# Optimization experiments

Measured on AMD Instinct MI355X. Metric: run time of the kernel, lower is better.

The kernel has to match this reference:

```python
import jax, jax.numpy as jnp
import numpy as np

N = 20000; E = 320000; B = 512
F_IN = 43; HID = 128; H = 4; C = 128  # TransformerConv: out_channels=128, heads=4 -> H*C=512
SCALE = float(1.0 / np.sqrt(C))


def _lin(key, nin, nout):
    k1, k2 = jax.random.split(key)
    W = jax.random.normal(k1, (nin, nout), jnp.float32) * 0.05
    b = jax.random.normal(k2, (nout,), jnp.float32) * 0.05
    return W, b


def setup_inputs() -> dict:
    key = jax.random.key(0)
    ks = jax.random.split(key, 64)
    inp = {}
    inp['x'] = jax.random.normal(ks[0], (N, F_IN), jnp.float32)
    inp['edge_index'] = jax.random.randint(ks[1], (2, E), 0, N, jnp.int32)
    inp['batch'] = jnp.sort(jax.random.randint(ks[2], (N,), 0, B, jnp.int32))
    i = 3
    for l, din in enumerate([F_IN, HID, HID], start=1):
        for nm in ['q', 'k', 'v', 's']:
            W, b = _lin(ks[i], din, H * C); i += 1
            inp['W%s%d' % (nm, l)] = W
            inp['b%s%d' % (nm, l)] = b
        W, b = _lin(ks[i], H * C, HID); i += 1
        inp['Wm%d' % l] = W; inp['bm%d' % l] = b
    inp['Wg1'], inp['bg1'] = _lin(ks[i], 2 * HID, 1024); i += 1
    inp['Wg2'], inp['bg2'] = _lin(ks[i], 1024, 512); i += 1
    inp['Wf1'], inp['bf1'] = _lin(ks[i], 512, 256); i += 1
    inp['Wf2'], inp['bf2'] = _lin(ks[i], 256, 1); i += 1
    return inp


def _tconv(x, src, dst, Wq, bq, Wk, bk, Wv, bv, Ws, bs):
    # PyG TransformerConv (concat=True, root_weight=True, eval -> no dropout)
    n = x.shape[0]
    q = (x @ Wq + bq).reshape(n, H, C)
    k = (x @ Wk + bk).reshape(n, H, C)
    v = (x @ Wv + bv).reshape(n, H, C)
    alpha = jnp.einsum('ehc,ehc->eh', q[dst], k[src]) * SCALE  # [E, H]
    amax = jax.ops.segment_max(alpha, dst, num_segments=n)
    amax = jnp.where(jnp.isfinite(amax), amax, 0.0)
    ex = jnp.exp(alpha - amax[dst])
    den = jax.ops.segment_sum(ex, dst, num_segments=n)
    w = ex / jnp.maximum(den[dst], 1e-16)  # segment softmax over incoming edges
    agg = jax.ops.segment_sum(w[:, :, None] * v[src], dst, num_segments=n)
    return agg.reshape(n, H * C) + x @ Ws + bs


def reference(x, edge_index, batch,
              Wq1, bq1, Wk1, bk1, Wv1, bv1, Ws1, bs1, Wm1, bm1,
              Wq2, bq2, Wk2, bk2, Wv2, bv2, Ws2, bs2, Wm2, bm2,
              Wq3, bq3, Wk3, bk3, Wv3, bv3, Ws3, bs3, Wm3, bm3,
              Wg1, bg1, Wg2, bg2, Wf1, bf1, Wf2, bf2):
    src, dst = edge_index[0], edge_index[1]
    layers = [
        (Wq1, bq1, Wk1, bk1, Wv1, bv1, Ws1, bs1, Wm1, bm1),
        (Wq2, bq2, Wk2, bk2, Wv2, bv2, Ws2, bs2, Wm2, bm2),
        (Wq3, bq3, Wk3, bk3, Wv3, bv3, Ws3, bs3, Wm3, bm3),
    ]
    h = x
    for (Wq, bq, Wk, bk, Wv, bv, Ws, bs, Wm, bm) in layers:
        h = jax.nn.relu(_tconv(h, src, dst, Wq, bq, Wk, bk, Wv, bv, Ws, bs) @ Wm + bm)
    # global max pool + global mean pool over graphs
    gm = jax.ops.segment_max(h, batch, num_segments=B)
    gm = jnp.where(jnp.isfinite(gm), gm, 0.0)
    cnt = jax.ops.segment_sum(jnp.ones((h.shape[0], 1), h.dtype), batch, num_segments=B)
    ga = jax.ops.segment_sum(h, batch, num_segments=B) / jnp.maximum(cnt, 1.0)
    g = jnp.concatenate([gm, ga], axis=1)  # [B, 256]
    g = jax.nn.relu(g @ Wg1 + bg1)
    g = jax.nn.relu(g @ Wg2 + bg2)
    g = jax.nn.relu(g @ Wf1 + bf1)
    return g @ Wf2 + bf2  # [B, 1]
```

## Files before the change

### kernel.cpp

```cpp
#include <hip/hip_runtime.h>
#include <hip/hip_bf16.h>
#include <hip/hip_fp16.h>
#include <math.h>

#define NN 20000
#define MPAD 20096
#define NE 320000
#define NB 512
#define FIN 43
#define HD 128
#define HC 512
#define ATT_SCALE 0.08838834764831843f

typedef __attribute__((ext_vector_type(8))) _Float16 f16x8v;
typedef __attribute__((ext_vector_type(8))) short short8v;
typedef __attribute__((ext_vector_type(4))) float f32x4v;
typedef _Float16 half2_t __attribute__((ext_vector_type(2)));

__device__ __forceinline__ void gload16(void* lds, const void* g) {
  __builtin_amdgcn_global_load_lds(
      (const __attribute__((address_space(1))) void*)g,
      (__attribute__((address_space(3))) void*)lds, 16, 0, 0);
}

__device__ __forceinline__ float dot2acc(half2_t a, half2_t b, float c) {
#if __has_builtin(__builtin_amdgcn_fdot2)
  return __builtin_amdgcn_fdot2(a, b, c, false);
#else
  return c + (float)a[0] * (float)b[0] + (float)a[1] * (float)b[1];
#endif
}

__global__ __launch_bounds__(256, 2) void gemm_qkv_kernel(
    const __half* __restrict__ A_, int ldA,
    const __half* __restrict__ B_,
    const float* __restrict__ bias,
    __half* __restrict__ qh16, __half* __restrict__ kvh,
    int M, int K)
{
  __shared__ _Float16 Ah[128 * 64], Bh[128 * 64];
  const _Float16* A = (const _Float16*)A_;
  const _Float16* B = (const _Float16*)B_;
  const int tid = threadIdx.x;
  const int w = tid >> 6, lane = tid & 63;
  const int rowBase = blockIdx.y * 128, colBase = blockIdx.x * 128;
  const int srow = lane >> 3;
  const int sw = ((lane & 7) ^ srow) << 3;
  const int lr = lane & 15, lg = lane >> 4;
  const int wr = w >> 1, wc = w & 1;

  f32x4v acc[4][4];
#pragma unroll
  for (int m = 0; m < 4; ++m)
#pragma unroll
    for (int n = 0; n < 4; ++n) acc[m][n] = (f32x4v){0.f, 0.f, 0.f, 0.f};

  for (int k0 = 0; k0 < K; k0 += 64) {
    if (k0) __syncthreads();
#pragma unroll
    for (int t = 0; t < 4; ++t) {
      int r0 = w * 32 + t * 8;
      size_t arow = (size_t)(rowBase + r0 + srow) * ldA + k0 + sw;
      size_t brow = (size_t)(colBase + r0 + srow) * K + k0 + sw;
      gload16(&Ah[r0 * 64], A + arow);
      gload16(&Bh[r0 * 64], B + brow);
    }
    __syncthreads();
#pragma unroll
    for (int kk = 0; kk < 2; ++kk) {
      f16x8v ah[4], bh[4];
      int cbase = ((kk * 4 + lg) ^ (lr & 7)) * 8;
#pragma unroll
      for (int m = 0; m < 4; ++m)
        ah[m] = *(const f16x8v*)&Ah[(wr * 64 + m * 16 + lr) * 64 + cbase];
#pragma unroll
      for (int n = 0; n < 4; ++n)
        bh[n] = *(const f16x8v*)&Bh[(wc * 64 + n * 16 + lr) * 64 + cbase];
#pragma unroll
      for (int m = 0; m < 4; ++m)
#pragma unroll
        for (int n = 0; n < 4; ++n)
          acc[m][n] = __builtin_amdgcn_mfma_f32_16x16x32_f16(ah[m], bh[n], acc[m][n], 0, 0, 0);
    }
  }
#pragma unroll
  for (int m = 0; m < 4; ++m) {
#pragma unroll
    for (int n = 0; n < 4; ++n) {
      int col = colBase + wc * 64 + n * 16 + lr;
      float bb = bias[col];
#pragma unroll
      for (int r = 0; r < 4; ++r) {
        int row = rowBase + wr * 64 + m * 16 + lg * 4 + r;
        if (row < M) {
          float v = acc[m][n][r] + bb;
          if (col < 512) {
            qh16[(size_t)row * 512 + col] = __float2half(v);
          } else if (col < 1024) {
            int cc = col - 512;
            kvh[(size_t)row * 1024 + (cc >> 7) * 256 + (cc & 127)] = __float2half(v);
          } else {
            int cc = col - 1024;
            kvh[(size_t)row * 1024 + (cc >> 7) * 256 + 128 + (cc & 127)] = __float2half(v);
          }
        }
      }
    }
  }
}

__global__ __launch_bounds__(256, 2) void gemm64_kernel(
    const __half* __restrict__ A_, int ldA, int Ksplit,
    const __half* __restrict__ A2_, int ldA2,
    const __half* __restrict__ B_,
    const float* __restrict__ bias,
    float* __restrict__ Y, int ldY,
    __half* __restrict__ Yh,
    int M, int K)
{
  __shared__ _Float16 Ah[64 * 64], Bh[128 * 64];
  const _Float16* B = (const _Float16*)B_;
  const int tid = threadIdx.x;
  const int w = tid >> 6, lane = tid & 63;
  const int rowBase = blockIdx.x * 64, colBase = blockIdx.y * 128;
  const int srow = lane >> 3;
  const int sw = ((lane & 7) ^ srow) << 3;
  const int lr = lane & 15, lg = lane >> 4;
  const int wr = w >> 1, wc = w & 1;

  f32x4v acc[2][4];
#pragma unroll
  for (int m = 0; m < 2; ++m)
#pragma unroll
    for (int n = 0; n < 4; ++n) acc[m][n] = (f32x4v){0.f, 0.f, 0.f, 0.f};

  for (int k0 = 0; k0 < K; k0 += 64) {
    if (k0) __syncthreads();
    const _Float16* sA;
    int ldS, kloc;
    if (k0 < Ksplit) { sA = (const _Float16*)A_;  ldS = ldA;  kloc = k0; }
    else             { sA = (const _Float16*)A2_; ldS = ldA2; kloc = k0 - Ksplit; }
#pragma unroll
    for (int t = 0; t < 2; ++t) {
      int r0 = w * 16 + t * 8;
      size_t arow = (size_t)(rowBase + r0 + srow) * ldS + kloc + sw;
      gload16(&Ah[r0 * 64], sA + arow);
    }
#pragma unroll
    for (int t = 0; t < 4; ++t) {
      int r0 = w * 32 + t * 8;
      size_t brow = (size_t)(colBase + r0 + srow) * K + k0 + sw;
      gload16(&Bh[r0 * 64], B + brow);
    }
    __syncthreads();
#pragma unroll
    for (int kk = 0; kk < 2; ++kk) {
      f16x8v ah[2], bh[4];
      int cbase = ((kk * 4 + lg) ^ (lr & 7)) * 8;
#pragma unroll
      for (int m = 0; m < 2; ++m)
        ah[m] = *(const f16x8v*)&Ah[(wr * 32 + m * 16 + lr) * 64 + cbase];
#pragma unroll
      for (int n = 0; n < 4; ++n)
        bh[n] = *(const f16x8v*)&Bh[(wc * 64 + n * 16 + lr) * 64 + cbase];
#pragma unroll
      for (int m = 0; m < 2; ++m)
#pragma unroll
        for (int n = 0; n < 4; ++n)
          acc[m][n] = __builtin_amdgcn_mfma_f32_16x16x32_f16(ah[m], bh[n], acc[m][n], 0, 0, 0);
    }
  }
#pragma unroll
  for (int m = 0; m < 2; ++m) {
#pragma unroll
    for (int n = 0; n < 4; ++n) {
      int col = colBase + wc * 64 + n * 16 + lr;
      float bb = bias[col];
#pragma unroll
      for (int r = 0; r < 4; ++r) {
        int row = rowBase + wr * 32 + m * 16 + lg * 4 + r;
        if (row < M) {
          float v = fmaxf(acc[m][n][r] + bb, 0.f);
          if (Y) Y[(size_t)row * ldY + col] = v;
          Yh[(size_t)row * ldY + col] = __float2half(v);
        }
      }
    }
  }
}

struct WsmArgs {
  const float* Ws[3];
  const float* Wm[3];
  const float* bs[3];
  const float* bm[3];
  __half* Wmx[3];
  float* bm2;
};

__global__ __launch_bounds__(256) void wsm_kernel(WsmArgs a)
{
  int idx = blockIdx.x * 256 + threadIdx.x;
  if (idx < 3 * 128 * 128) {
    int l = idx >> 14, r = idx & 16383;
    int n = r >> 7, d = r & 127;
    int K2pad = (l == 0) ? 64 : 128;
    if (d >= K2pad) return;
    int din = (l == 0) ? FIN : 128;
    float v = 0.f;
    if (d < din) {
      const float* ws = a.Ws[l] + (size_t)d * 512;
      const float* wm = a.Wm[l];
      for (int j = 0; j < 512; ++j) v += ws[j] * wm[(size_t)j * 128 + n];
    }
    int KP = 512 + K2pad;
    a.Wmx[l][(size_t)n * KP + 512 + d] = __float2half(v);
  } else {
    int r = idx - 3 * 128 * 128;
    if (r >= 384) return;
    int l = r >> 7, n = r & 127;
    float v = a.bm[l][n];
    const float* bs = a.bs[l];
    const float* wm = a.Wm[l];
    for (int j = 0; j < 512; ++j) v += bs[j] * wm[(size_t)j * 128 + n];
    a.bm2[l * 128 + n] = v;
  }
}

struct PackArgs {
  const float* W[9];
  const float* b[9];
  const float* Wm[3];
  const float *Wg1, *Wg2, *Wf1;
  __half* Wp[3];
  __half* Wmx[3];
  __half *Wg1p, *Wg2p, *Wf1p;
  float* bpack;
};

__global__ __launch_bounds__(256) void pack_all_kernel(PackArgs a)
{
  int idx = blockIdx.x * 256 + threadIdx.x;
  if (idx < 98304) {
    int n = idx >> 6, k = idx & 63;
    int mat = n >> 9, nn = n & 511;
    float v = (k < FIN) ? a.W[mat][(size_t)k * 512 + nn] : 0.f;
    a.Wp[0][idx] = __float2half(v);
  } else if (idx < 491520) {
    int rel = idx - 98304;
    int l = 1 + rel / 196608;
    int r2 = rel % 196608;
    int n = r2 >> 7, k = r2 & 127;
    int mat = n >> 9, nn = n & 511;
    a.Wp[l][r2] = __float2half(a.W[l * 3 + mat][(size_t)k * 512 + nn]);
  } else if (idx < 688128) {
    int rel = idx - 491520;
    int l = rel >> 16;
    int r2 = rel & 65535;
    int n = r2 >> 9, k = r2 & 511;
    int KP = (l == 0) ? 576 : 640;
    a.Wmx[l][(size_t)n * KP + k] = __float2half(a.Wm[l][(size_t)k * 128 + n]);
  } else if (idx < 692736) {
    int rel = idx - 688128;
    int l = rel / 1536, c = rel % 1536;
    a.bpack[rel] = a.b[l * 3 + (c >> 9)][c & 511];
  } else if (idx < 954880) {
    int rel = idx - 692736;
    int n = rel >> 8, k = rel & 255;
    a.Wg1p[rel] = __float2half(a.Wg1[(size_t)k * 1024 + n]);
  } else if (idx < 1479168) {
    int rel = idx - 954880;
    int n = rel >> 10, k = rel & 1023;
    a.Wg2p[rel] = __float2half(a.Wg2[(size_t)k * 512 + n]);
  } else if (idx < 1610240) {
    int rel = idx - 1479168;
    int n = rel >> 9, k = rel & 511;
    a.Wf1p[rel] = __float2half(a.Wf1[(size_t)k * 256 + n]);
  }
}

__global__ __launch_bounds__(256) void split_x_kernel(
    const float* __restrict__ x, __half* __restrict__ xh)
{
  int idx = blockIdx.x * 256 + threadIdx.x;
  if (idx >= NN * 64) return;
  int r = idx >> 6, c = idx & 63;
  float v = (c < FIN) ? x[(size_t)r * FIN + c] : 0.f;
  xh[idx] = __float2half(v);
}

__global__ __launch_bounds__(256) void count_kernel(const int* __restrict__ dst, int* __restrict__ cnt)
{
  int e = blockIdx.x * 256 + threadIdx.x;
  if (e < NE) atomicAdd(&cnt[dst[e]], 1);
}

__global__ __launch_bounds__(1024) void scan_kernel(const int* __restrict__ cnt, int* __restrict__ row_start)
{
  __shared__ int sums[1024];
  int t = threadIdx.x;
  const int per = (NN + 1023) / 1024;
  int beg = t * per;
  int end = beg + per; if (end > NN) end = NN; if (beg > NN) beg = NN;
  int s = 0;
  for (int i = beg; i < end; ++i) s += cnt[i];
  sums[t] = s;
  __syncthreads();
  for (int off = 1; off < 1024; off <<= 1) {
    int v = (t >= off) ? sums[t - off] : 0;
    __syncthreads();
    sums[t] += v;
    __syncthreads();
  }
  int prefix = (t == 0) ? 0 : sums[t - 1];
  for (int i = beg; i < end; ++i) { row_start[i] = prefix; prefix += cnt[i]; }
  if (t == 1023) row_start[NN] = prefix;
}

__global__ __launch_bounds__(256) void scatter_kernel(
    const int* __restrict__ src, const int* __restrict__ dst,
    const int* __restrict__ row_start,
    int* __restrict__ cursor, int* __restrict__ edge_list)
{
  int e = blockIdx.x * 256 + threadIdx.x;
  if (e < NE) {
    int d = dst[e];
    int p = atomicAdd(&cursor[d], 1);
    edge_list[row_start[d] + p] = src[e];
  }
}

__global__ __launch_bounds__(256) void attn_kernel(
    const __half* __restrict__ qh16, const __half* __restrict__ kvh,
    const int* __restrict__ row_start, const int* __restrict__ edge_list,
    __half* __restrict__ t0h)
{
  const int tid = threadIdx.x;
  const int w = tid >> 6, lane = tid & 63;
  const int node = blockIdx.x * 4 + w;
  const int hd = blockIdx.y;
  const int g4 = lane >> 4, sl = lane & 15;
  const int beg = row_start[node], cnt = row_start[node + 1] - beg;

  float4 qraw = *(const float4*)(qh16 + (size_t)node * 512 + hd * 128 + 8 * sl);
  const half2_t* qh = (const half2_t*)&qraw;

  float m = -INFINITY, den = 0.f;
  float a[8] = {0.f, 0.f, 0.f, 0.f, 0.f, 0.f, 0.f, 0.f};

  auto upd = [&](float p, const float4& vraw) {
    const __half2* vh = (const __half2*)&vraw;
    float2 f0 = __half22float2(vh[0]);
    float2 f1 = __half22float2(vh[1]);
    float2 f2 = __half22float2(vh[2]);
    float2 f3 = __half22float2(vh[3]);
    if (__builtin_expect(p > m + 8.f, 0)) {
      float c = __expf(m - p);
      den = den * c + 1.f;
      a[0] = a[0] * c + f0.x; a[1] = a[1] * c + f0.y;
      a[2] = a[2] * c + f1.x; a[3] = a[3] * c + f1.y;
      a[4] = a[4] * c + f2.x; a[5] = a[5] * c + f2.y;
      a[6] = a[6] * c + f3.x; a[7] = a[7] * c + f3.y;
      m = p;
    } else {
      float e = __expf(p - m);
      den += e;
      a[0] += e * f0.x; a[1] += e * f0.y;
      a[2] += e * f1.x; a[3] += e * f1.y;
      a[4] += e * f2.x; a[5] += e * f2.y;
      a[6] += e * f3.x; a[7] += e * f3.y;
    }
  };

  const int* el = edge_list + beg;
  for (int j = 4 * g4; j < cnt; j += 16) {
    bool h1 = (j + 1 < cnt), h2 = (j + 2 < cnt), h3 = (j + 3 < cnt);
    int s0 = el[j];
    int s1 = h1 ? el[j + 1] : s0;
    int s2 = h2 ? el[j + 2] : s0;
    int s3 = h3 ? el[j + 3] : s0;
    const __half* b0 = kvh + (size_t)s0 * 1024 + hd * 256 + 8 * sl;
    const __half* b1 = kvh + (size_t)s1 * 1024 + hd * 256 + 8 * sl;
    const __half* b2 = kvh + (size_t)s2 * 1024 + hd * 256 + 8 * sl;
    const __half* b3 = kvh + (size_t)s3 * 1024 + hd * 256 + 8 * sl;
    float4 k0 = *(const float4*)b0;
    float4 k1 = *(const float4*)b1;
    float4 k2 = *(const float4*)b2;
    float4 k3 = *(const float4*)b3;
    float4 v0 = *(const float4*)(b0 + 128);
    float4 v1 = *(const float4*)(b1 + 128);
    float4 v2 = *(const float4*)(b2 + 128);
    float4 v3 = *(const float4*)(b3 + 128);

    const half2_t* kh0 = (const half2_t*)&k0;
    const half2_t* kh1 = (const half2_t*)&k1;
    const half2_t* kh2 = (const half2_t*)&k2;
    const half2_t* kh3 = (const half2_t*)&k3;
    float p0 = 0.f, p1 = 0.f, p2 = 0.f, p3 = 0.f;
#pragma unroll
    for (int i = 0; i < 4; ++i) {
      p0 = dot2acc(qh[i], kh0[i], p0);
      p1 = dot2acc(qh[i], kh1[i], p1);
      p2 = dot2acc(qh[i], kh2[i], p2);
      p3 = dot2acc(qh[i], kh3[i], p3);
    }
#pragma unroll
    for (int off = 8; off >= 1; off >>= 1) {
      p0 += __shfl_xor(p0, off);
      p1 += __shfl_xor(p1, off);
      p2 += __shfl_xor(p2, off);
      p3 += __shfl_xor(p3, off);
    }
    p0 *= ATT_SCALE; p1 *= ATT_SCALE; p2 *= ATT_SCALE; p3 *= ATT_SCALE;
    upd(p0, v0);
    if (h1) upd(p1, v1);
    if (h2) upd(p2, v2);
    if (h3) upd(p3, v3);
  }

  float m2 = fmaxf(m, __shfl_xor(m, 16));
  float mAll = fmaxf(m2, __shfl_xor(m2, 32));
  float scale = (m == -INFINITY) ? 0.f : __expf(m - mAll);
  den *= scale;
  den += __shfl_xor(den, 16);
  den += __shfl_xor(den, 32);
#pragma unroll
  for (int i = 0; i < 8; ++i) {
    a[i] *= scale;
    a[i] += __shfl_xor(a[i], 16);
    a[i] += __shfl_xor(a[i], 32);
  }

  if (g4 == 0) {
    float inv = 1.f / fmaxf(den, 1e-16f);
    short8v o8;
#pragma unroll
    for (int i = 0; i < 8; ++i) {
      __half hv = __float2half(a[i] * inv);
      o8[i] = *(short*)&hv;
    }
    size_t o = (size_t)node * HC + hd * 128 + 8 * sl;
    *(short8v*)(t0h + o) = o8;
  }
}

__global__ __launch_bounds__(256) void pool_init_kernel(float* __restrict__ gm, float* __restrict__ gsum, int* __restrict__ gcnt)
{
  int i = blockIdx.x * 256 + threadIdx.x;
  if (i < NB * HD) { ((int*)gm)[i] = 0xFF800000; gsum[i] = 0.f; }
  if (i < NB) gcnt[i] = 0;
}

#define PN 32
__global__ __launch_bounds__(256) void pool_kernel(
    const float* __restrict__ h, const int* __restrict__ batch,
    float* __restrict__ gm, float* __restrict__ gsum, int* __restrict__ gcnt)
{
  __shared__ int sbatch[PN];
  const int base = blockIdx.x * PN;
  const int tid = threadIdx.x;
  if (tid < PN) {
    int n = base + tid;
    sbatch[tid] = (n < NN) ? batch[n] : -1;
  }
  __syncthreads();
  const int c = tid & 127;
  const int half = tid >> 7;
  const int i0 = half * (PN / 2), i1 = i0 + PN / 2;

  float sum = 0.f, mx = -INFINITY;
  int cur = sbatch[i0];
  bool any = false;
  for (int i = i0; i < i1; ++i) {
    int n = base + i;
    if (n >= NN) break;
    int b = sbatch[i];
    if (b != cur) {
      if (any) {
        atomicAdd(&gsum[(size_t)cur * HD + c], sum);
        atomicMax((int*)&gm[(size_t)cur * HD + c], __float_as_int(mx));
      }
      sum = 0.f; mx = -INFINITY; cur = b; any = false;
    }
    float val = h[(size_t)n * HD + c];
    sum += val; mx = fmaxf(mx, val);
    any = true;
  }
  if (any && cur >= 0) {
    atomicAdd(&gsum[(size_t)cur * HD + c], sum);
    atomicMax((int*)&gm[(size_t)cur * HD + c], __float_as_int(mx));
  }
  if (c == 0) {
    int cnt = 0; int cb = sbatch[i0];
    for (int i = i0; i < i1; ++i) {
      int n = base + i;
      if (n >= NN) break;
      if (sbatch[i] != cb) {
        if (cnt > 0 && cb >= 0) atomicAdd(&gcnt[cb], cnt);
        cnt = 0; cb = sbatch[i];
      }
      cnt++;
    }
    if (cnt > 0 && cb >= 0) atomicAdd(&gcnt[cb], cnt);
  }
}

__global__ __launch_bounds__(256) void pool_finalize_kernel(
    const float* __restrict__ gm, const float* __restrict__ gsum,
    const int* __restrict__ gcnt, __half* __restrict__ gh)
{
  int idx = blockIdx.x * 256 + threadIdx.x;
  if (idx >= NB * HD) return;
  int b = idx >> 7, c = idx & 127;
  float mv = gm[idx];
  if (mv < -1e30f) mv = 0.f;
  float cf = (float)gcnt[b];
  float av = gsum[idx] / fmaxf(cf, 1.f);
  size_t o0 = (size_t)b * 256 + c;
  gh[o0] = __float2half(mv);
  gh[o0 + 128] = __float2half(av);
}

__global__ __launch_bounds__(256) void head4_kernel(
    const float* __restrict__ g3, const float* __restrict__ Wf2,
    const float* __restrict__ bf2, float* __restrict__ out)
{
  int w = threadIdx.x >> 6, lane = threadIdx.x & 63;
  int row = blockIdx.x * 4 + w;
  const float* r = g3 + (size_t)row * 256;
  float p = r[lane] * Wf2[lane] + r[64 + lane] * Wf2[64 + lane]
          + r[128 + lane] * Wf2[128 + lane] + r[192 + lane] * Wf2[192 + lane];
#pragma unroll
  for (int off = 32; off >= 1; off >>= 1) p += __shfl_xor(p, off);
  if (lane == 0) out[row] = p + bf2[0];
}

extern "C" void kernel_launch(void* const* d_in, const int* in_sizes, int n_in,
                              void* d_out, int out_size, void* d_ws, size_t ws_size,
                              hipStream_t stream)
{
  const float* x = (const float*)d_in[0];
  const int* edge_index = (const int*)d_in[1];
  const int* batch = (const int*)d_in[2];
  const int* src = edge_index;
  const int* dstv = edge_index + NE;

  const float *Wq[3], *bq[3], *Wk[3], *bk[3], *Wv[3], *bv[3], *Wsk[3], *bsk[3], *Wm[3], *bm[3];
  int base = 3;
  for (int l = 0; l < 3; ++l) {
    Wq[l]  = (const float*)d_in[base + 0]; bq[l]  = (const float*)d_in[base + 1];
    Wk[l]  = (const float*)d_in[base + 2]; bk[l]  = (const float*)d_in[base + 3];
    Wv[l]  = (const float*)d_in[base + 4]; bv[l]  = (const float*)d_in[base + 5];
    Wsk[l] = (const float*)d_in[base + 6]; bsk[l] = (const float*)d_in[base + 7];
    Wm[l]  = (const float*)d_in[base + 8]; bm[l]  = (const float*)d_in[base + 9];
    base += 10;
  }
  const float* Wg1 = (const float*)d_in[33]; const float* bg1 = (const float*)d_in[34];
  const float* Wg2 = (const float*)d_in[35]; const float* bg2 = (const float*)d_in[36];
  const float* Wf1 = (const float*)d_in[37]; const float* bf1 = (const float*)d_in[38];
  const float* Wf2 = (const float*)d_in[39]; const float* bf2 = (const float*)d_in[40];

  char* p = (char*)d_ws;
  auto alloc = [&](size_t bytes) { char* r = p; p += (bytes + 255) & ~(size_t)255; return r; };
  __half* qh16 = (__half*)alloc((size_t)MPAD * 512 * 2);
  __half* kvh  = (__half*)alloc((size_t)MPAD * 1024 * 2);
  float* h    = (float*)alloc((size_t)NN * HD * 4);
  __half* t0h = (__half*)alloc((size_t)MPAD * HC * 2);
  __half* hA  = (__half*)alloc((size_t)MPAD * HD * 2);
  __half* hB  = (__half*)alloc((size_t)MPAD * HD * 2);
  __half* xh  = (__half*)alloc((size_t)MPAD * 64 * 2);
  __half *Wp[3], *Wmx[3];
  Wp[0] = (__half*)alloc((size_t)1536 * 64 * 2);
  for (int l = 1; l < 3; ++l) Wp[l] = (__half*)alloc((size_t)1536 * 128 * 2);
  for (int l = 0; l < 3; ++l) {
    int KP = (l == 0) ? 576 : 640;
    Wmx[l] = (__half*)alloc((size_t)128 * KP * 2);
  }
  __half* Wg1p = (__half*)alloc((size_t)1024 * 256 * 2);
  __half* Wg2p = (__half*)alloc((size_t)512 * 1024 * 2);
  __half* Wf1p = (__half*)alloc((size_t)256 * 512 * 2);
  float* bpack = (float*)alloc(3 * 1536 * 4);
  float* bm2   = (float*)alloc(3 * 128 * 4);
  float* gm   = (float*)alloc((size_t)NB * HD * 4);
  float* gsum = (float*)alloc((size_t)NB * HD * 4);
  __half* gh  = (__half*)alloc((size_t)NB * 256 * 2);
  __half* g1h = (__half*)alloc((size_t)NB * 1024 * 2);
  __half* g2h = (__half*)alloc((size_t)NB * 512 * 2);
  float* g3   = (float*)alloc((size_t)NB * 256 * 4);
  __half* g3h = (__half*)alloc((size_t)NB * 256 * 2);
  int* icnt      = (int*)alloc(NN * 4);
  int* cursor    = (int*)alloc(NN * 4);
  int* row_start = (int*)alloc((NN + 1) * 4);
  int* edge_list = (int*)alloc((size_t)NE * 4);
  int* gcnt      = (int*)alloc(NB * 4);

  const int GR128 = (NN + 127) / 128;
  const int GR64  = (NN + 63) / 64;

  PackArgs pa;
  for (int l = 0; l < 3; ++l) {
    pa.W[l * 3 + 0] = Wq[l];  pa.W[l * 3 + 1] = Wk[l];  pa.W[l * 3 + 2] = Wv[l];
    pa.b[l * 3 + 0] = bq[l];  pa.b[l * 3 + 1] = bk[l];  pa.b[l * 3 + 2] = bv[l];
    pa.Wm[l] = Wm[l];
    pa.Wp[l] = Wp[l];
    pa.Wmx[l] = Wmx[l];
  }
  pa.Wg1 = Wg1; pa.Wg2 = Wg2; pa.Wf1 = Wf1;
  pa.Wg1p = Wg1p; pa.Wg2p = Wg2p; pa.Wf1p = Wf1p;
  pa.bpack = bpack;
  pack_all_kernel<<<(1610240 + 255) / 256, 256, 0, stream>>>(pa);

  WsmArgs wa;
  for (int l = 0; l < 3; ++l) {
    wa.Ws[l] = Wsk[l]; wa.Wm[l] = Wm[l]; wa.bs[l] = bsk[l]; wa.bm[l] = bm[l];
    wa.Wmx[l] = Wmx[l];
  }
  wa.bm2 = bm2;
  wsm_kernel<<<(3 * 128 * 128 + 384 + 255) / 256, 256, 0, stream>>>(wa);

  hipMemsetAsync(icnt, 0, sizeof(int) * NN, stream);
  hipMemsetAsync(cursor, 0, sizeof(int) * NN, stream);
  count_kernel<<<(NE + 255) / 256, 256, 0, stream>>>(dstv, icnt);
  scan_kernel<<<1, 1024, 0, stream>>>(icnt, row_start);
  scatter_kernel<<<(NE + 255) / 256, 256, 0, stream>>>(src, dstv, row_start, cursor, edge_list);

  split_x_kernel<<<(NN * 64 + 255) / 256, 256, 0, stream>>>(x, xh);

  const __half* Ain = xh;
  int KpadIn = 64;
  for (int l = 0; l < 3; ++l) {
    __half* Hout = (l & 1) ? hB : hA;

    gemm_qkv_kernel<<<dim3(12, GR128), 256, 0, stream>>>(
        Ain, KpadIn, Wp[l], bpack + l * 1536, qh16, kvh, NN, KpadIn);

    attn_kernel<<<dim3(NN / 4, 4), 256, 0, stream>>>(
        qh16, kvh, row_start, edge_list, t0h);

    gemm64_kernel<<<dim3(GR64, 1), 256, 0, stream>>>(
        t0h, HC, 512, Ain, KpadIn,
        Wmx[l], bm2 + l * 128,
        (l == 2) ? h : nullptr, HD, Hout, NN, 512 + KpadIn);

    Ain = Hout; KpadIn = 128;
  }

  pool_init_kernel<<<(NB * HD + 255) / 256, 256, 0, stream>>>(gm, gsum, gcnt);
  pool_kernel<<<(NN + PN - 1) / PN, 256, 0, stream>>>(h, batch, gm, gsum, gcnt);
  pool_finalize_kernel<<<(NB * HD + 255) / 256, 256, 0, stream>>>(gm, gsum, gcnt, gh);

  gemm64_kernel<<<dim3(8, 8), 256, 0, stream>>>(
      gh, 256, 256, gh, 256, Wg1p, bg1, nullptr, 1024, g1h, NB, 256);
  gemm64_kernel<<<dim3(8, 4), 256, 0, stream>>>(
      g1h, 1024, 1024, g1h, 1024, Wg2p, bg2, nullptr, 512, g2h, NB, 1024);
  gemm64_kernel<<<dim3(8, 2), 256, 0, stream>>>(
      g2h, 512, 512, g2h, 512, Wf1p, bf1, g3, 256, g3h, NB, 512);
  head4_kernel<<<NB / 4, 256, 0, stream>>>(g3, Wf2, bf2, (float*)d_out);
}
```

Baseline: 510.9 us.

## Merge setup kernels, pool from fp16 activations, drop pool init and fp32 output

Folds weight packing, the Ws·Wm precomposition and the x fp16 conversion into one setup kernel, and replaces the pool init kernel with a single memset that relies on ReLU outputs being non-negative (max init 0). Pooling now reads the fp16 final activations, so the last GEMM no longer writes an fp32 copy. Attention loads of q and edge indices use nontemporal hints. This cuts launch count and memory traffic, but pooling from fp16 values adds rounding error compared with the fp32 path.

```diff
diff --git a/kernel.cpp b/kernel.cpp
--- a/kernel.cpp
+++ b/kernel.cpp
@@ -189,56 +189,28 @@
   }
 }
 
-struct WsmArgs {
-  const float* Ws[3];
-  const float* Wm[3];
-  const float* bs[3];
-  const float* bm[3];
-  __half* Wmx[3];
-  float* bm2;
-};
-
-__global__ __launch_bounds__(256) void wsm_kernel(WsmArgs a)
-{
-  int idx = blockIdx.x * 256 + threadIdx.x;
-  if (idx < 3 * 128 * 128) {
-    int l = idx >> 14, r = idx & 16383;
-    int n = r >> 7, d = r & 127;
-    int K2pad = (l == 0) ? 64 : 128;
-    if (d >= K2pad) return;
-    int din = (l == 0) ? FIN : 128;
-    float v = 0.f;
-    if (d < din) {
-      const float* ws = a.Ws[l] + (size_t)d * 512;
-      const float* wm = a.Wm[l];
-      for (int j = 0; j < 512; ++j) v += ws[j] * wm[(size_t)j * 128 + n];
-    }
-    int KP = 512 + K2pad;
-    a.Wmx[l][(size_t)n * KP + 512 + d] = __float2half(v);
-  } else {
-    int r = idx - 3 * 128 * 128;
-    if (r >= 384) return;
-    int l = r >> 7, n = r & 127;
-    float v = a.bm[l][n];
-    const float* bs = a.bs[l];
-    const float* wm = a.Wm[l];
-    for (int j = 0; j < 512; ++j) v += bs[j] * wm[(size_t)j * 128 + n];
-    a.bm2[l * 128 + n] = v;
-  }
-}
-
-struct PackArgs {
+struct SetupArgs {
   const float* W[9];
   const float* b[9];
   const float* Wm[3];
+  const float* Ws[3];
+  const float* bs[3];
+  const float* bm[3];
   const float *Wg1, *Wg2, *Wf1;
+  const float* x;
   __half* Wp[3];
   __half* Wmx[3];
   __half *Wg1p, *Wg2p, *Wf1p;
   float* bpack;
+  float* bm2;
+  __half* xh;
 };
 
-__global__ __launch_bounds__(256) void pack_all_kernel(PackArgs a)
+#define SEG_PACK 1610240
+#define SEG_WSM  (SEG_PACK + 49536)
+#define SEG_END  (SEG_WSM + NN * 64)
+
+__global__ __launch_bounds__(256) void setup_kernel(SetupArgs a)
 {
   int idx = blockIdx.x * 256 + threadIdx.x;
   if (idx < 98304) {
@@ -272,21 +244,42 @@
     int rel = idx - 954880;
     int n = rel >> 10, k = rel & 1023;
     a.Wg2p[rel] = __float2half(a.Wg2[(size_t)k * 512 + n]);
-  } else if (idx < 1610240) {
+  } else if (idx < SEG_PACK) {
     int rel = idx - 1479168;
     int n = rel >> 9, k = rel & 511;
     a.Wf1p[rel] = __float2half(a.Wf1[(size_t)k * 256 + n]);
-  }
-}
-
-__global__ __launch_bounds__(256) void split_x_kernel(
-    const float* __restrict__ x, __half* __restrict__ xh)
-{
-  int idx = blockIdx.x * 256 + threadIdx.x;
-  if (idx >= NN * 64) return;
-  int r = idx >> 6, c = idx & 63;
-  float v = (c < FIN) ? x[(size_t)r * FIN + c] : 0.f;
-  xh[idx] = __float2half(v);
+  } else if (idx < SEG_WSM) {
+    int r = idx - SEG_PACK;
+    if (r < 49152) {
+      int l = r >> 14, r2 = r & 16383;
+      int n = r2 >> 7, d = r2 & 127;
+      int K2pad = (l == 0) ? 64 : 128;
+      if (d >= K2pad) return;
+      int din = (l == 0) ? FIN : 128;
+      float v = 0.f;
+      if (d < din) {
+        const float* ws = a.Ws[l] + (size_t)d * 512;
+        const float* wm = a.Wm[l];
+        for (int j = 0; j < 512; ++j) v += ws[j] * wm[(size_t)j * 128 + n];
+      }
+      int KP = 512 + K2pad;
+      a.Wmx[l][(size_t)n * KP + 512 + d] = __float2half(v);
+    } else {
+      int r2 = r - 49152;
+      if (r2 >= 384) return;
+      int l = r2 >> 7, n = r2 & 127;
+      float v = a.bm[l][n];
+      const float* bs = a.bs[l];
+      const float* wm = a.Wm[l];
+      for (int j = 0; j < 512; ++j) v += bs[j] * wm[(size_t)j * 128 + n];
+      a.bm2[l * 128 + n] = v;
+    }
+  } else if (idx < SEG_END) {
+    int rel = idx - SEG_WSM;
+    int rr = rel >> 6, c = rel & 63;
+    float v = (c < FIN) ? a.x[(size_t)rr * FIN + c] : 0.f;
+    a.xh[rel] = __float2half(v);
+  }
 }
 
 __global__ __launch_bounds__(256) void count_kernel(const int* __restrict__ dst, int* __restrict__ cnt)
@@ -342,7 +335,8 @@
   const int g4 = lane >> 4, sl = lane & 15;
   const int beg = row_start[node], cnt = row_start[node + 1] - beg;
 
-  float4 qraw = *(const float4*)(qh16 + (size_t)node * 512 + hd * 128 + 8 * sl);
+  f32x4v qraw = __builtin_nontemporal_load(
+      (const f32x4v*)(qh16 + (size_t)node * 512 + hd * 128 + 8 * sl));
   const half2_t* qh = (const half2_t*)&qraw;
 
   float m = -INFINITY, den = 0.f;
@@ -375,10 +369,10 @@
   const int* el = edge_list + beg;
   for (int j = 4 * g4; j < cnt; j += 16) {
     bool h1 = (j + 1 < cnt), h2 = (j + 2 < cnt), h3 = (j + 3 < cnt);
-    int s0 = el[j];
-    int s1 = h1 ? el[j + 1] : s0;
-    int s2 = h2 ? el[j + 2] : s0;
-    int s3 = h3 ? el[j + 3] : s0;
+    int s0 = __builtin_nontemporal_load(el + j);
+    int s1 = h1 ? __builtin_nontemporal_load(el + j + 1) : s0;
+    int s2 = h2 ? __builtin_nontemporal_load(el + j + 2) : s0;
+    int s3 = h3 ? __builtin_nontemporal_load(el + j + 3) : s0;
     const __half* b0 = kvh + (size_t)s0 * 1024 + hd * 256 + 8 * sl;
     const __half* b1 = kvh + (size_t)s1 * 1024 + hd * 256 + 8 * sl;
     const __half* b2 = kvh + (size_t)s2 * 1024 + hd * 256 + 8 * sl;
@@ -444,16 +438,9 @@
   }
 }
 
-__global__ __launch_bounds__(256) void pool_init_kernel(float* __restrict__ gm, float* __restrict__ gsum, int* __restrict__ gcnt)
-{
-  int i = blockIdx.x * 256 + threadIdx.x;
-  if (i < NB * HD) { ((int*)gm)[i] = 0xFF800000; gsum[i] = 0.f; }
-  if (i < NB) gcnt[i] = 0;
-}
-
 #define PN 32
 __global__ __launch_bounds__(256) void pool_kernel(
-    const float* __restrict__ h, const int* __restrict__ batch,
+    const __half* __restrict__ h, const int* __restrict__ batch,
     float* __restrict__ gm, float* __restrict__ gsum, int* __restrict__ gcnt)
 {
   __shared__ int sbatch[PN];
@@ -468,7 +455,7 @@
   const int half = tid >> 7;
   const int i0 = half * (PN / 2), i1 = i0 + PN / 2;
 
-  float sum = 0.f, mx = -INFINITY;
+  float sum = 0.f, mx = 0.f;
   int cur = sbatch[i0];
   bool any = false;
   for (int i = i0; i < i1; ++i) {
@@ -480,9 +467,9 @@
         atomicAdd(&gsum[(size_t)cur * HD + c], sum);
         atomicMax((int*)&gm[(size_t)cur * HD + c], __float_as_int(mx));
       }
-      sum = 0.f; mx = -INFINITY; cur = b; any = false;
-    }
-    float val = h[(size_t)n * HD + c];
+      sum = 0.f; mx = 0.f; cur = b; any = false;
+    }
+    float val = __half2float(h[(size_t)n * HD + c]);
     sum += val; mx = fmaxf(mx, val);
     any = true;
   }
@@ -513,7 +500,6 @@
   if (idx >= NB * HD) return;
   int b = idx >> 7, c = idx & 127;
   float mv = gm[idx];
-  if (mv < -1e30f) mv = 0.f;
   float cf = (float)gcnt[b];
   float av = gsum[idx] / fmaxf(cf, 1.f);
   size_t o0 = (size_t)b * 256 + c;
@@ -564,7 +550,6 @@
   auto alloc = [&](size_t bytes) { char* r = p; p += (bytes + 255) & ~(size_t)255; return r; };
   __half* qh16 = (__half*)alloc((size_t)MPAD * 512 * 2);
   __half* kvh  = (__half*)alloc((size_t)MPAD * 1024 * 2);
-  float* h    = (float*)alloc((size_t)NN * HD * 4);
   __half* t0h = (__half*)alloc((size_t)MPAD * HC * 2);
   __half* hA  = (__half*)alloc((size_t)MPAD * HD * 2);
   __half* hB  = (__half*)alloc((size_t)MPAD * HD * 2);
@@ -581,50 +566,41 @@
   __half* Wf1p = (__half*)alloc((size_t)256 * 512 * 2);
   float* bpack = (float*)alloc(3 * 1536 * 4);
   float* bm2   = (float*)alloc(3 * 128 * 4);
-  float* gm   = (float*)alloc((size_t)NB * HD * 4);
-  float* gsum = (float*)alloc((size_t)NB * HD * 4);
+  float* gm   = (float*)alloc((size_t)NB * HD * 4 * 2 + NB * 4);
+  float* gsum = gm + (size_t)NB * HD;
+  int* gcnt   = (int*)(gsum + (size_t)NB * HD);
   __half* gh  = (__half*)alloc((size_t)NB * 256 * 2);
   __half* g1h = (__half*)alloc((size_t)NB * 1024 * 2);
   __half* g2h = (__half*)alloc((size_t)NB * 512 * 2);
   float* g3   = (float*)alloc((size_t)NB * 256 * 4);
   __half* g3h = (__half*)alloc((size_t)NB * 256 * 2);
-  int* icnt      = (int*)alloc(NN * 4);
-  int* cursor    = (int*)alloc(NN * 4);
+  int* icnt      = (int*)alloc((size_t)2 * NN * 4);
+  int* cursor    = icnt + NN;
   int* row_start = (int*)alloc((NN + 1) * 4);
   int* edge_list = (int*)alloc((size_t)NE * 4);
-  int* gcnt      = (int*)alloc(NB * 4);
 
   const int GR128 = (NN + 127) / 128;
   const int GR64  = (NN + 63) / 64;
 
-  PackArgs pa;
+  (void)hipMemsetAsync(icnt, 0, (size_t)2 * NN * 4, stream);
+  (void)hipMemsetAsync(gm, 0, (size_t)NB * HD * 4 * 2 + NB * 4, stream);
+
+  SetupArgs sa;
   for (int l = 0; l < 3; ++l) {
-    pa.W[l * 3 + 0] = Wq[l];  pa.W[l * 3 + 1] = Wk[l];  pa.W[l * 3 + 2] = Wv[l];
-    pa.b[l * 3 + 0] = bq[l];  pa.b[l * 3 + 1] = bk[l];  pa.b[l * 3 + 2] = bv[l];
-    pa.Wm[l] = Wm[l];
-    pa.Wp[l] = Wp[l];
-    pa.Wmx[l] = Wmx[l];
-  }
-  pa.Wg1 = Wg1; pa.Wg2 = Wg2; pa.Wf1 = Wf1;
-  pa.Wg1p = Wg1p; pa.Wg2p = Wg2p; pa.Wf1p = Wf1p;
-  pa.bpack = bpack;
-  pack_all_kernel<<<(1610240 + 255) / 256, 256, 0, stream>>>(pa);
-
-  WsmArgs wa;
-  for (int l = 0; l < 3; ++l) {
-    wa.Ws[l] = Wsk[l]; wa.Wm[l] = Wm[l]; wa.bs[l] = bsk[l]; wa.bm[l] = bm[l];
-    wa.Wmx[l] = Wmx[l];
-  }
-  wa.bm2 = bm2;
-  wsm_kernel<<<(3 * 128 * 128 + 384 + 255) / 256, 256, 0, stream>>>(wa);
-
-  hipMemsetAsync(icnt, 0, sizeof(int) * NN, stream);
-  hipMemsetAsync(cursor, 0, sizeof(int) * NN, stream);
+    sa.W[l * 3 + 0] = Wq[l];  sa.W[l * 3 + 1] = Wk[l];  sa.W[l * 3 + 2] = Wv[l];
+    sa.b[l * 3 + 0] = bq[l];  sa.b[l * 3 + 1] = bk[l];  sa.b[l * 3 + 2] = bv[l];
+    sa.Wm[l] = Wm[l]; sa.Ws[l] = Wsk[l]; sa.bs[l] = bsk[l]; sa.bm[l] = bm[l];
+    sa.Wp[l] = Wp[l]; sa.Wmx[l] = Wmx[l];
+  }
+  sa.Wg1 = Wg1; sa.Wg2 = Wg2; sa.Wf1 = Wf1;
+  sa.x = x;
+  sa.Wg1p = Wg1p; sa.Wg2p = Wg2p; sa.Wf1p = Wf1p;
+  sa.bpack = bpack; sa.bm2 = bm2; sa.xh = xh;
+  setup_kernel<<<(SEG_END + 255) / 256, 256, 0, stream>>>(sa);
+
   count_kernel<<<(NE + 255) / 256, 256, 0, stream>>>(dstv, icnt);
   scan_kernel<<<1, 1024, 0, stream>>>(icnt, row_start);
   scatter_kernel<<<(NE + 255) / 256, 256, 0, stream>>>(src, dstv, row_start, cursor, edge_list);
-
-  split_x_kernel<<<(NN * 64 + 255) / 256, 256, 0, stream>>>(x, xh);
 
   const __half* Ain = xh;
   int KpadIn = 64;
@@ -640,13 +616,13 @@
     gemm64_kernel<<<dim3(GR64, 1), 256, 0, stream>>>(
         t0h, HC, 512, Ain, KpadIn,
         Wmx[l], bm2 + l * 128,
-        (l == 2) ? h : nullptr, HD, Hout, NN, 512 + KpadIn);
+        nullptr, HD, Hout, NN, 512 + KpadIn);
 
     Ain = Hout; KpadIn = 128;
   }
-
-  pool_init_kernel<<<(NB * HD + 255) / 256, 256, 0, stream>>>(gm, gsum, gcnt);
-  pool_kernel<<<(NN + PN - 1) / PN, 256, 0, stream>>>(h, batch, gm, gsum, gcnt);
+  const __half* hFinal = hA;
+
+  pool_kernel<<<(NN + PN - 1) / PN, 256, 0, stream>>>(hFinal, batch, gm, gsum, gcnt);
   pool_finalize_kernel<<<(NB * HD + 255) / 256, 256, 0, stream>>>(gm, gsum, gcnt, gh);
 
   gemm64_kernel<<<dim3(8, 8), 256, 0, stream>>>(
```

New measurement: 552.0 us. +8.1%, slower.
